# Optimization experiments

Measured on AMD Instinct MI355X. Metric: run time of the kernel, lower is better.

The kernel has to match this reference:

```python
import jax, jax.numpy as jnp
import numpy as np

TEMP = 0.3  # softmax temperature used in load-balance loss


def setup_inputs() -> dict:
    key = jax.random.key(0)
    k1, k2 = jax.random.split(key)
    num_tokens, d_model, num_expert = 16384, 4096, 128
    inp = jax.random.normal(k1, (num_tokens, d_model), dtype=jnp.float32)
    wg = jax.random.normal(k2, (num_expert, d_model), dtype=jnp.float32) * (1.0 / np.sqrt(d_model))
    return {"inp": inp, "wg": wg, "top_k": 2}


def reference(inp, wg, top_k):
    # Gate logits: [T, E] = [T, D] @ [D, E]
    logits = jnp.einsum("td,ed->te", inp, wg)
    # Top-k selection + softmax over the k selected logits
    top_vals, top_idx = jax.lax.top_k(logits, top_k)  # [T, k]
    gate_score = jax.nn.softmax(top_vals, axis=-1)    # [T, k]
    # Load-balance loss (stored as self.loss in torch; returned here)
    T, E = logits.shape
    probs = jax.nn.softmax(logits / TEMP, axis=-1)    # [T, E]
    mask = jax.nn.one_hot(top_idx[:, 0], E, dtype=probs.dtype) * (E / T)
    me = jnp.sum(probs, axis=0)                       # [E]
    ce = jnp.sum(mask, axis=0)                        # [E]
    loss = jnp.sum(me * ce) / T
    return top_idx, gate_score, loss
```

## Files before the change

kernel.cpp:

```cpp
#include <hip/hip_runtime.h>

typedef _Float16 half8 __attribute__((ext_vector_type(8)));
typedef float floatx4 __attribute__((ext_vector_type(4)));

#define NTOK 16384
#define DM   4096
#define NE   128
#define MT   32
#define BK   64
#define NITER (DM / BK)
#define NBLK (NTOK / MT)
#define TEMP 0.3f
#define CSTRIDE 528
#define ABUF (8 * CSTRIDE)
#define BUFSZ (2 * ABUF)
#define LSTRIDE 33

__global__ void pack_b_kernel(const float* __restrict__ wg, _Float16* __restrict__ Bp) {
    int gtid = blockIdx.x * blockDim.x + threadIdx.x;
    int l  = gtid & 63;
    int tg = gtid >> 6;
    int g  = tg & 7;
    int kc = tg >> 3;
    const float* src = wg + (size_t)(g * 16 + (l & 15)) * DM + kc * 32 + (l >> 4) * 8;
    float4 v0 = *(const float4*)src;
    float4 v1 = *(const float4*)(src + 4);
    float f[8] = {v0.x, v0.y, v0.z, v0.w, v1.x, v1.y, v1.z, v1.w};
    half8 h1, h2;
#pragma unroll
    for (int j = 0; j < 8; j++) {
        h1[j] = (_Float16)f[j];
        h2[j] = (_Float16)((f[j] - (float)h1[j]) * 2048.0f);
    }
    char* dst = (char*)Bp + (size_t)tg * 2048 + l * 16;
    *(half8*)dst = h1;
    *(half8*)(dst + 1024) = h2;
}

__device__ __forceinline__ void stage_write(unsigned char* base, unsigned off,
                                            float4 v0, float4 v1) {
    float f[8] = {v0.x, v0.y, v0.z, v0.w, v1.x, v1.y, v1.z, v1.w};
    half8 h1, h2;
#pragma unroll
    for (int j = 0; j < 8; j++) {
        h1[j] = (_Float16)f[j];
        h2[j] = (_Float16)((f[j] - (float)h1[j]) * 2048.0f);
    }
    *(half8*)(base + off) = h1;
    *(half8*)(base + ABUF + off) = h2;
}

__launch_bounds__(256, 2)
__global__ void moe_fused_kernel(const float* __restrict__ A,
                                 const _Float16* __restrict__ Bp,
                                 float* __restrict__ out,
                                 float* __restrict__ mece) {
    __shared__ __align__(16) unsigned char smem[2 * BUFSZ];
    __shared__ float tmax[MT], tscale[MT];
    float* LG = (float*)smem;
    const int tid  = threadIdx.x;
    const int wave = tid >> 6;
    const int lane = tid & 63;
    const int quad = lane >> 4;
    const int lrow = lane & 15;
    const int tok0 = blockIdx.x * MT;

    const int srow = tid >> 3;
    const int schunk = tid & 7;
    const float* aptr = A + (size_t)(tok0 + srow) * DM + schunk * 8;
    const unsigned swoff = schunk * CSTRIDE + srow * 16;
    const unsigned aroff = quad * CSTRIDE + lrow * 16;

    const char* bB = (const char*)Bp + (wave * 2) * 2048 + lane * 16;

    floatx4 accm[2][2], accc[2][2];
#pragma unroll
    for (int r = 0; r < 2; r++)
#pragma unroll
        for (int c = 0; c < 2; c++) {
            accm[r][c] = (floatx4){0.f, 0.f, 0.f, 0.f};
            accc[r][c] = (floatx4){0.f, 0.f, 0.f, 0.f};
        }

    {
        float4 v0 = *(const float4*)aptr;
        float4 v1 = *(const float4*)(aptr + 4);
        stage_write(smem, swoff, v0, v1);
    }
    __syncthreads();

    for (int it = 0; it < NITER; ++it) {
        float4 n0, n1;
        if (it < NITER - 1) {
            const float* p = aptr + (it + 1) * BK;
            n0 = *(const float4*)p;
            n1 = *(const float4*)(p + 4);
        }
        unsigned char* cb = smem + (it & 1) * BUFSZ;
        const char* bit = bB + (size_t)it * 32768;

#pragma unroll
        for (int ks = 0; ks < 2; ++ks) {
            half8 b1f[2], b2f[2], a1[2], a2[2];
#pragma unroll
            for (int c = 0; c < 2; c++) {
                b1f[c] = *(const half8*)(bit + ks * 16384 + c * 2048);
                b2f[c] = *(const half8*)(bit + ks * 16384 + c * 2048 + 1024);
            }
#pragma unroll
            for (int r = 0; r < 2; r++) {
                a1[r] = *(const half8*)(cb + ks * 2112 + r * 256 + aroff);
                a2[r] = *(const half8*)(cb + ABUF + ks * 2112 + r * 256 + aroff);
            }
#pragma unroll
            for (int r = 0; r < 2; r++)
#pragma unroll
                for (int c = 0; c < 2; c++) {
                    accm[r][c] = __builtin_amdgcn_mfma_f32_16x16x32_f16(a1[r], b1f[c], accm[r][c], 0, 0, 0);
                    accc[r][c] = __builtin_amdgcn_mfma_f32_16x16x32_f16(a1[r], b2f[c], accc[r][c], 0, 0, 0);
                    accc[r][c] = __builtin_amdgcn_mfma_f32_16x16x32_f16(a2[r], b1f[c], accc[r][c], 0, 0, 0);
                }
        }
        if (it < NITER - 1)
            stage_write(smem + ((it + 1) & 1) * BUFSZ, swoff, n0, n1);
        __syncthreads();
    }

#pragma unroll
    for (int r = 0; r < 2; r++)
#pragma unroll
        for (int c = 0; c < 2; c++) {
            const int e  = wave * 32 + c * 16 + lrow;
            const int tt = r * 16 + quad * 4;
#pragma unroll
            for (int g = 0; g < 4; g++)
                LG[e * LSTRIDE + tt + g] = accm[r][c][g] + accc[r][c][g] * (1.0f / 2048.0f);
        }
    __syncthreads();

    if (tid < MT) {
        const int t = tid;
        float m1 = -1e30f, m2 = -1e30f;
        int i1 = 0, i2 = 0;
        for (int e = 0; e < NE; e++) {
            float v = LG[e * LSTRIDE + t];
            if (v > m1) { m2 = m1; i2 = i1; m1 = v; i1 = e; }
            else if (v > m2) { m2 = v; i2 = e; }
        }
        float s = 0.f;
        for (int e = 0; e < NE; e++)
            s += __expf((LG[e * LSTRIDE + t] - m1) * (1.0f / TEMP));
        tmax[t] = m1;
        tscale[t] = 1.0f / s;

        const int tg = tok0 + t;
        out[tg * 2 + 0] = (float)i1;
        out[tg * 2 + 1] = (float)i2;
        float d = __expf(m2 - m1);
        float g1 = 1.0f / (1.0f + d);
        out[2 * NTOK + tg * 2 + 0] = g1;
        out[2 * NTOK + tg * 2 + 1] = d * g1;

        atomicAdd(&mece[NE + i1], 1.0f);
    }
    __syncthreads();

    if (tid < NE) {
        const int e = tid;
        float s = 0.f;
#pragma unroll
        for (int t = 0; t < MT; t++)
            s += __expf((LG[e * LSTRIDE + t] - tmax[t]) * (1.0f / TEMP)) * tscale[t];
        atomicAdd(&mece[e], s);
    }
}

__global__ void finalize_kernel(const float* __restrict__ mece, float* __restrict__ out) {
    __shared__ float w2[2];
    const int tid = threadIdx.x;
    float v = mece[tid] * mece[NE + tid] * ((float)NE / (float)NTOK);
#pragma unroll
    for (int off = 32; off; off >>= 1) v += __shfl_down(v, off);
    if ((tid & 63) == 0) w2[tid >> 6] = v;
    __syncthreads();
    if (tid == 0) out[4 * NTOK] = (w2[0] + w2[1]) / (float)NTOK;
}

extern "C" void kernel_launch(void* const* d_in, const int* in_sizes, int n_in,
                              void* d_out, int out_size, void* d_ws, size_t ws_size,
                              hipStream_t stream) {
    (void)in_sizes; (void)n_in; (void)out_size; (void)ws_size;
    const float* inp = (const float*)d_in[0];
    const float* wg  = (const float*)d_in[1];
    float* out = (float*)d_out;

    _Float16* Bp = (_Float16*)d_ws;
    float* mece  = (float*)((char*)d_ws + (2u << 20));

    hipMemsetAsync(mece, 0, 2 * NE * sizeof(float), stream);
    pack_b_kernel<<<256, 256, 0, stream>>>(wg, Bp);
    moe_fused_kernel<<<NBLK, 256, 0, stream>>>(inp, Bp, out, mece);
    finalize_kernel<<<1, NE, 0, stream>>>(mece, out);
}
```

Measured before the change: 465.9 us.

## Split K dimension across two blocks per token tile with last-block reduction

Splits the 4096-wide reduction into two halves handled by separate blocks, doubling the grid to 1024 blocks so more work is available across the CUs, and raises launch bounds to 4 blocks per CU. Each block writes its partial logits to a workspace buffer, and an atomic counter per tile picks the second-finishing block, which adds the other partial and runs the top-k, softmax and loss epilogue. This adds global traffic for the partial sums, fences and atomics, and relies on the workspace being large enough for the partial buffers.

```diff
diff --git a/kernel.cpp b/kernel.cpp
--- a/kernel.cpp
+++ b/kernel.cpp
@@ -8,8 +8,11 @@
 #define NE   128
 #define MT   32
 #define BK   64
-#define NITER (DM / BK)
-#define NBLK (NTOK / MT)
+#define KSPLIT 2
+#define KHALF (DM / KSPLIT)
+#define NITER (KHALF / BK)
+#define NTILE (NTOK / MT)
+#define NBLK  (NTILE * KSPLIT)
 #define TEMP 0.3f
 #define CSTRIDE 528
 #define ABUF (8 * CSTRIDE)
@@ -50,28 +53,33 @@
     *(half8*)(base + ABUF + off) = h2;
 }
 
-__launch_bounds__(256, 2)
+__launch_bounds__(256, 4)
 __global__ void moe_fused_kernel(const float* __restrict__ A,
                                  const _Float16* __restrict__ Bp,
                                  float* __restrict__ out,
-                                 float* __restrict__ mece) {
+                                 float* __restrict__ mece,
+                                 float* __restrict__ part,
+                                 int* __restrict__ cnt) {
     __shared__ __align__(16) unsigned char smem[2 * BUFSZ];
     __shared__ float tmax[MT], tscale[MT];
+    __shared__ int sOld;
     float* LG = (float*)smem;
     const int tid  = threadIdx.x;
     const int wave = tid >> 6;
     const int lane = tid & 63;
     const int quad = lane >> 4;
     const int lrow = lane & 15;
-    const int tok0 = blockIdx.x * MT;
+    const int tile = blockIdx.x & (NTILE - 1);
+    const int half = blockIdx.x >> 9;
+    const int tok0 = tile * MT;
 
     const int srow = tid >> 3;
     const int schunk = tid & 7;
-    const float* aptr = A + (size_t)(tok0 + srow) * DM + schunk * 8;
+    const float* aptr = A + (size_t)(tok0 + srow) * DM + half * KHALF + schunk * 8;
     const unsigned swoff = schunk * CSTRIDE + srow * 16;
     const unsigned aroff = quad * CSTRIDE + lrow * 16;
 
-    const char* bB = (const char*)Bp + (wave * 2) * 2048 + lane * 16;
+    const char* bB = (const char*)Bp + ((size_t)half << 20) + (wave * 2) * 2048 + lane * 16;
 
     floatx4 accm[2][2], accc[2][2];
 #pragma unroll
@@ -126,15 +134,43 @@
         __syncthreads();
     }
 
+    floatx4 v[2][2];
+#pragma unroll
+    for (int r = 0; r < 2; r++)
+#pragma unroll
+        for (int c = 0; c < 2; c++)
+#pragma unroll
+            for (int g = 0; g < 4; g++)
+                v[r][c][g] = accm[r][c][g] + accc[r][c][g] * (1.0f / 2048.0f);
+
+    float* pslot = part + ((size_t)(half * NTILE + tile)) * (MT * NE);
 #pragma unroll
     for (int r = 0; r < 2; r++)
 #pragma unroll
         for (int c = 0; c < 2; c++) {
-            const int e  = wave * 32 + c * 16 + lrow;
-            const int tt = r * 16 + quad * 4;
+            const int e = wave * 32 + c * 16 + lrow;
+            const int t = r * 16 + quad * 4;
+            *(floatx4*)(pslot + e * MT + t) = v[r][c];
+        }
+    __threadfence();
+    __syncthreads();
+    if (tid == 0)
+        sOld = __hip_atomic_fetch_add(&cnt[tile], 1, __ATOMIC_ACQ_REL, __HIP_MEMORY_SCOPE_AGENT);
+    __syncthreads();
+    if (sOld != 1) return;
+    __threadfence();
+
+    const float* oslot = part + ((size_t)((half ^ 1) * NTILE + tile)) * (MT * NE);
+#pragma unroll
+    for (int r = 0; r < 2; r++)
+#pragma unroll
+        for (int c = 0; c < 2; c++) {
+            const int e = wave * 32 + c * 16 + lrow;
+            const int t = r * 16 + quad * 4;
+            floatx4 o = *(const floatx4*)(oslot + e * MT + t);
 #pragma unroll
             for (int g = 0; g < 4; g++)
-                LG[e * LSTRIDE + tt + g] = accm[r][c][g] + accc[r][c][g] * (1.0f / 2048.0f);
+                LG[e * LSTRIDE + t + g] = v[r][c][g] + o[g];
         }
     __syncthreads();
 
@@ -143,9 +179,9 @@
         float m1 = -1e30f, m2 = -1e30f;
         int i1 = 0, i2 = 0;
         for (int e = 0; e < NE; e++) {
-            float v = LG[e * LSTRIDE + t];
-            if (v > m1) { m2 = m1; i2 = i1; m1 = v; i1 = e; }
-            else if (v > m2) { m2 = v; i2 = e; }
+            float vv = LG[e * LSTRIDE + t];
+            if (vv > m1) { m2 = m1; i2 = i1; m1 = vv; i1 = e; }
+            else if (vv > m2) { m2 = vv; i2 = e; }
         }
         float s = 0.f;
         for (int e = 0; e < NE; e++)
@@ -196,9 +232,11 @@
 
     _Float16* Bp = (_Float16*)d_ws;
     float* mece  = (float*)((char*)d_ws + (2u << 20));
-
-    hipMemsetAsync(mece, 0, 2 * NE * sizeof(float), stream);
+    int*   cnt   = (int*)(mece + 2 * NE);
+    float* part  = (float*)((char*)d_ws + (4u << 20));
+
+    hipMemsetAsync(mece, 0, 2 * NE * sizeof(float) + NTILE * sizeof(int), stream);
     pack_b_kernel<<<256, 256, 0, stream>>>(wg, Bp);
-    moe_fused_kernel<<<NBLK, 256, 0, stream>>>(inp, Bp, out, mece);
+    moe_fused_kernel<<<NBLK, 256, 0, stream>>>(inp, Bp, out, mece, part, cnt);
     finalize_kernel<<<1, NE, 0, stream>>>(mece, out);
 }
```

After: 617.5 us. 1.33x slower.

## Split gate GEMM over K into four partial tiles with a separate top-k epilogue

Applied to the files above, without the earlier changes.

The gate GEMM is split along the model dimension into four slices, so the grid grows from 512 to 2048 blocks and the launch bound rises to 8 blocks per CU. The aim is more waves resident per CU to hide global-load latency on the streamed input. Each block writes its partial logits to a workspace buffer. A new epilogue kernel sums the four partials, does top-2 selection and the softmax/load-balance sums over 64-token tiles, and uses a shared-memory histogram to cut global atomics. The cost is an extra kernel launch plus writing and re-reading roughly 32 MB of partial logits, and it assumes the workspace is large enough.

```diff
diff --git a/kernel.cpp b/kernel.cpp
--- a/kernel.cpp
+++ b/kernel.cpp
@@ -8,13 +8,18 @@
 #define NE   128
 #define MT   32
 #define BK   64
-#define NITER (DM / BK)
-#define NBLK (NTOK / MT)
+#define KSPLIT 4
+#define KHALF (DM / KSPLIT)
+#define NITER (KHALF / BK)
+#define NTILE (NTOK / MT)
+#define NBLK  (NTILE * KSPLIT)
+#define ET   64
+#define NBLK_EPI (NTOK / ET)
 #define TEMP 0.3f
 #define CSTRIDE 528
 #define ABUF (8 * CSTRIDE)
 #define BUFSZ (2 * ABUF)
-#define LSTRIDE 33
+#define PSLOT (MT * NE)
 
 __global__ void pack_b_kernel(const float* __restrict__ wg, _Float16* __restrict__ Bp) {
     int gtid = blockIdx.x * blockDim.x + threadIdx.x;
@@ -50,28 +55,27 @@
     *(half8*)(base + ABUF + off) = h2;
 }
 
-__launch_bounds__(256, 2)
-__global__ void moe_fused_kernel(const float* __restrict__ A,
-                                 const _Float16* __restrict__ Bp,
-                                 float* __restrict__ out,
-                                 float* __restrict__ mece) {
+__launch_bounds__(256, 8)
+__global__ void moe_gemm_kernel(const float* __restrict__ A,
+                                const _Float16* __restrict__ Bp,
+                                float* __restrict__ part) {
     __shared__ __align__(16) unsigned char smem[2 * BUFSZ];
-    __shared__ float tmax[MT], tscale[MT];
-    float* LG = (float*)smem;
     const int tid  = threadIdx.x;
     const int wave = tid >> 6;
     const int lane = tid & 63;
     const int quad = lane >> 4;
     const int lrow = lane & 15;
-    const int tok0 = blockIdx.x * MT;
+    const int tile = blockIdx.x & (NTILE - 1);
+    const int half = blockIdx.x >> 9;
+    const int tok0 = tile * MT;
 
     const int srow = tid >> 3;
     const int schunk = tid & 7;
-    const float* aptr = A + (size_t)(tok0 + srow) * DM + schunk * 8;
+    const float* aptr = A + (size_t)(tok0 + srow) * DM + half * KHALF + schunk * 8;
     const unsigned swoff = schunk * CSTRIDE + srow * 16;
     const unsigned aroff = quad * CSTRIDE + lrow * 16;
 
-    const char* bB = (const char*)Bp + (wave * 2) * 2048 + lane * 16;
+    const char* bB = (const char*)Bp + ((size_t)half << 19) + (wave * 2) * 2048 + lane * 16;
 
     floatx4 accm[2][2], accc[2][2];
 #pragma unroll
@@ -126,52 +130,89 @@
         __syncthreads();
     }
 
+    float* pslot = part + ((size_t)half * NTILE + tile) * PSLOT;
 #pragma unroll
     for (int r = 0; r < 2; r++)
 #pragma unroll
         for (int c = 0; c < 2; c++) {
-            const int e  = wave * 32 + c * 16 + lrow;
-            const int tt = r * 16 + quad * 4;
+            floatx4 v;
 #pragma unroll
             for (int g = 0; g < 4; g++)
-                LG[e * LSTRIDE + tt + g] = accm[r][c][g] + accc[r][c][g] * (1.0f / 2048.0f);
-        }
-    __syncthreads();
-
-    if (tid < MT) {
+                v[g] = accm[r][c][g] + accc[r][c][g] * (1.0f / 2048.0f);
+            const int e = wave * 32 + c * 16 + lrow;
+            const int t = r * 16 + quad * 4;
+            *(floatx4*)(pslot + e * MT + t) = v;
+        }
+}
+
+__global__ void topk_kernel(const float* __restrict__ part,
+                            float* __restrict__ out,
+                            float* __restrict__ mece) {
+    __shared__ float LG[NE * 68];
+    __shared__ float tmax[ET], tscale[ET];
+    __shared__ int hist[NE];
+    const int tid = threadIdx.x;
+    const int t0  = blockIdx.x * ET;
+
+    {
+        const int q = tid & 3;
+        const size_t gtile = (size_t)(blockIdx.x * 2 + (q >> 1));
+#pragma unroll
+        for (int pass = 0; pass < 2; pass++) {
+            const int e = (tid >> 2) + pass * 64;
+            const size_t boff = gtile * PSLOT + e * MT + (q & 1) * 16;
+            float* dst = LG + e * 68 + q * 16;
+#pragma unroll
+            for (int j = 0; j < 16; j += 4) {
+                float4 s0 = *(const float4*)(part + 0 * NTILE * PSLOT + boff + j);
+                float4 s1 = *(const float4*)(part + 1 * NTILE * PSLOT + boff + j);
+                float4 s2 = *(const float4*)(part + 2 * NTILE * PSLOT + boff + j);
+                float4 s3 = *(const float4*)(part + 3 * NTILE * PSLOT + boff + j);
+                float4 s = {s0.x + s1.x + s2.x + s3.x,
+                            s0.y + s1.y + s2.y + s3.y,
+                            s0.z + s1.z + s2.z + s3.z,
+                            s0.w + s1.w + s2.w + s3.w};
+                *(float4*)(dst + j) = s;
+            }
+        }
+    }
+    if (tid < NE) hist[tid] = 0;
+    __syncthreads();
+
+    if (tid < ET) {
         const int t = tid;
         float m1 = -1e30f, m2 = -1e30f;
         int i1 = 0, i2 = 0;
         for (int e = 0; e < NE; e++) {
-            float v = LG[e * LSTRIDE + t];
+            float v = LG[e * 68 + t];
             if (v > m1) { m2 = m1; i2 = i1; m1 = v; i1 = e; }
             else if (v > m2) { m2 = v; i2 = e; }
         }
         float s = 0.f;
         for (int e = 0; e < NE; e++)
-            s += __expf((LG[e * LSTRIDE + t] - m1) * (1.0f / TEMP));
+            s += __expf((LG[e * 68 + t] - m1) * (1.0f / TEMP));
         tmax[t] = m1;
         tscale[t] = 1.0f / s;
-
-        const int tg = tok0 + t;
+        atomicAdd(&hist[i1], 1);
+
+        const int tg = t0 + t;
         out[tg * 2 + 0] = (float)i1;
         out[tg * 2 + 1] = (float)i2;
         float d = __expf(m2 - m1);
         float g1 = 1.0f / (1.0f + d);
         out[2 * NTOK + tg * 2 + 0] = g1;
         out[2 * NTOK + tg * 2 + 1] = d * g1;
-
-        atomicAdd(&mece[NE + i1], 1.0f);
     }
     __syncthreads();
 
     if (tid < NE) {
         const int e = tid;
         float s = 0.f;
-#pragma unroll
-        for (int t = 0; t < MT; t++)
-            s += __expf((LG[e * LSTRIDE + t] - tmax[t]) * (1.0f / TEMP)) * tscale[t];
+#pragma unroll 4
+        for (int t = 0; t < ET; t++)
+            s += __expf((LG[e * 68 + t] - tmax[t]) * (1.0f / TEMP)) * tscale[t];
         atomicAdd(&mece[e], s);
+        atomicAdd(&mece[NE + e], (float)hist[e]);
     }
 }
 
@@ -196,9 +237,11 @@
 
     _Float16* Bp = (_Float16*)d_ws;
     float* mece  = (float*)((char*)d_ws + (2u << 20));
+    float* part  = (float*)((char*)d_ws + (4u << 20));
 
     hipMemsetAsync(mece, 0, 2 * NE * sizeof(float), stream);
     pack_b_kernel<<<256, 256, 0, stream>>>(wg, Bp);
-    moe_fused_kernel<<<NBLK, 256, 0, stream>>>(inp, Bp, out, mece);
+    moe_gemm_kernel<<<NBLK, 256, 0, stream>>>(inp, Bp, part);
+    topk_kernel<<<NBLK_EPI, 256, 0, stream>>>(part, out, mece);
     finalize_kernel<<<1, NE, 0, stream>>>(mece, out);
 }
```

Measured after the change: 561.9 us. 1.21x slower.
